# Kernel optimization log

Hardware: AMD Instinct MI355X
Metric: run time of the kernel (lower is better)

Reference implementation:

```python
import jax, jax.numpy as jnp
import numpy as np


def setup_inputs() -> dict:
    key = jax.random.key(0)
    ks = jax.random.split(key, 12)
    B, IN, H = 4096, 512, 1024
    s = lambda k, shape, scale: jax.random.normal(k, shape, dtype=jnp.float32) * scale
    inp = {
        "inputs": s(ks[0], (B, IN), 1.0),
        "h0": s(ks[1], (B, H), 1.0),
        "c0": s(ks[2], (B, H), 1.0),
        "ts": jax.random.uniform(ks[3], (B, 2), dtype=jnp.float32),
        "w_ih": s(ks[4], (4 * H, IN), 1.0 / np.sqrt(IN)),
        "w_hh": s(ks[5], (4 * H, H), 1.0 / np.sqrt(H)),
        "b_ih": s(ks[6], (4 * H,), 1.0 / np.sqrt(H)),
        "b_hh": s(ks[7], (4 * H,), 1.0 / np.sqrt(H)),
        "w1": s(ks[8], (H, H), 1.0 / np.sqrt(H)),
        "b1": s(ks[9], (H,), 1.0 / np.sqrt(H)),
        "w2": s(ks[10], (H, H), 1.0 / np.sqrt(H)),
        "b2": s(ks[11], (H,), 1.0 / np.sqrt(H)),
    }
    return inp


def _lstm_cell(x, h, c, w_ih, w_hh, b_ih, b_hh):
    # gates: [B, 4H] in PyTorch (i, f, g, o) order
    gates = x @ w_ih.T + h @ w_hh.T + b_ih + b_hh
    i, f, g, o = jnp.split(gates, 4, axis=-1)
    i, f, o = jax.nn.sigmoid(i), jax.nn.sigmoid(f), jax.nn.sigmoid(o)
    g = jnp.tanh(g)
    c_new = f * c + i * g
    h_new = o * jnp.tanh(c_new)
    return h_new, c_new


def reference(inputs, h0, c0, ts, w_ih, w_hh, b_ih, b_hh, w1, b1, w2, b2):
    # Two stacked LSTMCell applications sharing the same weights
    h, c = _lstm_cell(inputs, h0, c0, w_ih, w_hh, b_ih, b_hh)
    h, c = _lstm_cell(inputs, h, c, w_ih, w_hh, b_ih, b_hh)

    # Autonomous ODE func: Linear -> Tanh -> Linear
    f = lambda y: jnp.tanh(y @ w1.T + b1) @ w2.T + b2

    # One RK4 step per sample from ts[:,0] to ts[:,1] (batched, no python loop)
    dt = (ts[:, 1] - ts[:, 0])[:, None]  # [B, 1]
    k1 = f(h)
    k2 = f(h + 0.5 * dt * k1)
    k3 = f(h + 0.5 * dt * k2)
    k4 = f(h + dt * k3)
    ht = h + (dt / 6.0) * (k1 + 2.0 * k2 + 2.0 * k3 + k4)
    return (ht, c)
```

## Files before the change

kernel.cpp:

```cpp
#include <hip/hip_runtime.h>

typedef short short8 __attribute__((ext_vector_type(8)));
typedef float f32x4 __attribute__((ext_vector_type(4)));
typedef unsigned short u16x8 __attribute__((ext_vector_type(8)));

#define B_DIM 4096
#define IN_DIM 512
#define H_DIM 1024
#define KCAT 1536

__device__ __forceinline__ float bs2f(unsigned short s) {
    return __uint_as_float(((unsigned int)s) << 16);
}
__device__ __forceinline__ unsigned short f2bs(float f) {
    unsigned int u = __float_as_uint(f);
    u += 0x7fff + ((u >> 16) & 1);
    return (unsigned short)(u >> 16);
}
__device__ __forceinline__ float sigm(float x) { return 1.0f / (1.0f + __expf(-x)); }
__device__ __forceinline__ float ftanh(float x) { return 1.0f - 2.0f / (__expf(2.0f * x) + 1.0f); }

__device__ __forceinline__ int gperm(int r) {
    int g = r >> 10, j = r & 1023;
    return ((j >> 4) << 6) + (g << 4) + (j & 15);
}

#define T0 262144
#define T1 786432
#define T2 1048576
#define T3 1572864
#define T4 1703936
#define T5 1835008
__device__ __forceinline__ u16x8 cvt8(const float* __restrict__ in, long i) {
    float4 a = *(const float4*)(in + i);
    float4 b = *(const float4*)(in + i + 4);
    u16x8 o;
    o[0] = f2bs(a.x); o[1] = f2bs(a.y); o[2] = f2bs(a.z); o[3] = f2bs(a.w);
    o[4] = f2bs(b.x); o[5] = f2bs(b.y); o[6] = f2bs(b.z); o[7] = f2bs(b.w);
    return o;
}
__global__ __launch_bounds__(256) void pack_all(const float* __restrict__ x,
                                                const float* __restrict__ h0,
                                                const float* __restrict__ wih,
                                                const float* __restrict__ whh,
                                                const float* __restrict__ w1,
                                                const float* __restrict__ w2,
                                                unsigned short* __restrict__ xb,
                                                unsigned short* __restrict__ hb0,
                                                unsigned short* __restrict__ wcat,
                                                unsigned short* __restrict__ w116,
                                                unsigned short* __restrict__ w216) {
    long g = (long)blockIdx.x * 256 + threadIdx.x;
    if (g < T0) {
        long i = g * 8;
        *(u16x8*)(xb + i) = cvt8(x, i);
    } else if (g < T1) {
        long i = (g - T0) * 8;
        *(u16x8*)(hb0 + i) = cvt8(h0, i);
    } else if (g < T2) {
        long i = (g - T1) * 8;
        int r = (int)(i / IN_DIM), c = (int)(i % IN_DIM);
        *(u16x8*)(wcat + (size_t)gperm(r) * KCAT + c) = cvt8(wih, i);
    } else if (g < T3) {
        long i = (g - T2) * 8;
        int r = (int)(i / H_DIM), c = (int)(i % H_DIM);
        *(u16x8*)(wcat + (size_t)gperm(r) * KCAT + IN_DIM + c) = cvt8(whh, i);
    } else if (g < T4) {
        long i = (g - T3) * 8;
        *(u16x8*)(w116 + i) = cvt8(w1, i);
    } else if (g < T5) {
        long i = (g - T4) * 8;
        *(u16x8*)(w216 + i) = cvt8(w2, i);
    }
}

__global__ __launch_bounds__(256) void prep_small(const float* __restrict__ bih,
                                                  const float* __restrict__ bhh,
                                                  const float* __restrict__ ts,
                                                  float* __restrict__ bsum,
                                                  float* __restrict__ dtv,
                                                  int n4h, int nb) {
    int i = blockIdx.x * blockDim.x + threadIdx.x;
    if (i < n4h) bsum[gperm(i)] = bih[i] + bhh[i];
    if (i < nb)  dtv[i] = ts[2 * i + 1] - ts[2 * i];
}

#define NT8 (KCAT / 32)

__global__ __launch_bounds__(512) void gemm8(
    const unsigned short* __restrict__ xb,
    const unsigned short* __restrict__ hb,
    const unsigned short* __restrict__ W,
    const float* __restrict__ bias,
    unsigned short* __restrict__ h_out,
    float* __restrict__ c_out,
    const float* __restrict__ c_in) {
    __shared__ unsigned short lA[3][256 * 32];
    __shared__ unsigned short lB[3][256 * 32];
    const int t = threadIdx.x;
    const int lane = t & 63;
    const int wave = t >> 6;
    const int wm = (wave >> 2) * 128;
    const int wn = (wave & 3) * 64;
    const int fr = lane & 15;
    const int kb = lane >> 4;
    const int tile_m = blockIdx.y * 256;
    const int tile_n = blockIdx.x * 256;

    f32x4 acc[8][4];
    #pragma unroll
    for (int i = 0; i < 8; ++i)
        #pragma unroll
        for (int j = 0; j < 4; ++j)
            acc[i][j] = (f32x4){0.f, 0.f, 0.f, 0.f};

    auto stageA = [&](int kt) {
        const int buf = kt % 3;
        #pragma unroll
        for (int j = 0; j < 2; ++j) {
            int idx = j * 512 + t;
            int row = idx >> 2;
            int g = idx & 3;
            int gs = g ^ ((row >> 1) & 3);
            int kk = kt * 32 + gs * 8;
            const unsigned short* src = (kk < IN_DIM)
                ? xb + (size_t)(tile_m + row) * IN_DIM + kk
                : hb + (size_t)(tile_m + row) * H_DIM + (kk - IN_DIM);
            __builtin_amdgcn_global_load_lds(
                (__attribute__((address_space(1))) void*)src,
                (__attribute__((address_space(3))) void*)(&lA[buf][row * 32 + g * 8]), 16, 0, 0);
        }
    };
    auto stageB = [&](int kt) {
        const int buf = kt % 3;
        #pragma unroll
        for (int j = 0; j < 2; ++j) {
            int idx = j * 512 + t;
            int row = idx >> 2;
            int g = idx & 3;
            int gs = g ^ ((row >> 1) & 3);
            int kk = kt * 32 + gs * 8;
            __builtin_amdgcn_global_load_lds(
                (__attribute__((address_space(1))) void*)(W + (size_t)(tile_n + row) * KCAT + kk),
                (__attribute__((address_space(3))) void*)(&lB[buf][row * 32 + g * 8]), 16, 0, 0);
        }
    };

    stageA(0); stageB(0);
    stageA(1); stageB(1);

    for (int kt = 0; kt < NT8; ++kt) {
        const int buf = kt % 3;
        if (kt + 1 < NT8) asm volatile("s_waitcnt vmcnt(4)" ::: "memory");
        else              asm volatile("s_waitcnt vmcnt(0)" ::: "memory");
        __builtin_amdgcn_s_barrier();
        asm volatile("" ::: "memory");
        short8 bfr[4], af[8];
        #pragma unroll
        for (int j = 0; j < 4; ++j) {
            int brow = wn + j * 16 + fr;
            bfr[j] = *(const short8*)&lB[buf][brow * 32 + (kb ^ ((brow >> 1) & 3)) * 8];
        }
        #pragma unroll
        for (int i = 0; i < 8; ++i) {
            int arow = wm + i * 16 + fr;
            af[i] = *(const short8*)&lA[buf][arow * 32 + (kb ^ ((arow >> 1) & 3)) * 8];
        }
        __builtin_amdgcn_s_setprio(1);
        #pragma unroll
        for (int i = 0; i < 8; ++i)
            #pragma unroll
            for (int j = 0; j < 4; ++j)
                acc[i][j] = __builtin_amdgcn_mfma_f32_16x16x32_bf16(af[i], bfr[j], acc[i][j], 0, 0, 0);
        __builtin_amdgcn_s_setprio(0);
        if (kt + 2 < NT8) { stageA(kt + 2); stageB(kt + 2); }
        asm volatile("" ::: "memory");
    }

    const int jbase = ((tile_n + wn) >> 6) << 4;
    float bv[4];
    #pragma unroll
    for (int g = 0; g < 4; ++g) bv[g] = bias[tile_n + wn + g * 16 + fr];
    #pragma unroll
    for (int i = 0; i < 8; ++i) {
        #pragma unroll
        for (int r = 0; r < 4; ++r) {
            const int m = tile_m + wm + i * 16 + kb * 4 + r;
            const int j = jbase + fr;
            float ig = sigm(acc[i][0][r] + bv[0]);
            float fg = sigm(acc[i][1][r] + bv[1]);
            float gg = ftanh(acc[i][2][r] + bv[2]);
            float og = sigm(acc[i][3][r] + bv[3]);
            float cin = c_in[(size_t)m * H_DIM + j];
            float cn = fg * cin + ig * gg;
            float hn = og * ftanh(cn);
            h_out[(size_t)m * H_DIM + j] = f2bs(hn);
            c_out[(size_t)m * H_DIM + j] = cn;
        }
    }
}

#define BKt 32

template <int EPI, int BM, int BN>
__global__ __launch_bounds__(256) void gemm2(
    const unsigned short* __restrict__ A1,
    const unsigned short* __restrict__ W,
    const int M, const int N, const int K,
    const float* __restrict__ bias,
    unsigned short* __restrict__ outb,
    float* __restrict__ outf,
    const unsigned short* __restrict__ hmat,
    const float* __restrict__ dtv,
    float* __restrict__ S,
    unsigned short* __restrict__ ynext,
    const float alpha, const float cw, const int first) {
    constexpr int WM = BM / 2;
    constexpr int WN = BN / 2;
    constexpr int MR = WM / 16;
    constexpr int NR = WN / 16;
    constexpr int ALOADS = BM * BKt / 8 / 256;
    constexpr int BLOADS = BN * BKt / 8 / 256;
    constexpr int LIF = ALOADS + BLOADS;

    __shared__ unsigned short lA[3][BM * BKt];
    __shared__ unsigned short lB[3][BN * BKt];
    const int t = threadIdx.x;
    const int lane = t & 63;
    const int wave = t >> 6;
    const int wm = (wave >> 1) * WM;
    const int wn = (wave & 1) * WN;
    const int fr = lane & 15;
    const int kb = lane >> 4;
    const int tile_m = blockIdx.y * BM;
    const int tile_n = blockIdx.x * BN;

    f32x4 acc[MR][NR];
    #pragma unroll
    for (int i = 0; i < MR; ++i)
        #pragma unroll
        for (int j = 0; j < NR; ++j)
            acc[i][j] = (f32x4){0.f, 0.f, 0.f, 0.f};

    const unsigned short* aptr1 = A1 + (size_t)tile_m * K;
    const unsigned short* wptr  = W + (size_t)tile_n * K;

    auto stage = [&](int kt) {
        const int buf = kt % 3;
        const int k0 = kt * BKt;
        #pragma unroll
        for (int j = 0; j < ALOADS; ++j) {
            int idx = j * 256 + t;
            int row = idx >> 2;
            int col = ((idx & 3) ^ ((row >> 1) & 3)) * 8;
            __builtin_amdgcn_global_load_lds(
                (__attribute__((address_space(1))) void*)(aptr1 + (size_t)row * K + k0 + col),
                (__attribute__((address_space(3))) void*)(&lA[buf][idx * 8]), 16, 0, 0);
        }
        #pragma unroll
        for (int j = 0; j < BLOADS; ++j) {
            int idx = j * 256 + t;
            int row = idx >> 2;
            int col = ((idx & 3) ^ ((row >> 1) & 3)) * 8;
            __builtin_amdgcn_global_load_lds(
                (__attribute__((address_space(1))) void*)(wptr + (size_t)row * K + k0 + col),
                (__attribute__((address_space(3))) void*)(&lB[buf][idx * 8]), 16, 0, 0);
        }
    };

    const int NT = K / BKt;
    stage(0);
    if (NT > 1) stage(1);
    for (int kt = 0; kt < NT; ++kt) {
        const int buf = kt % 3;
        if (kt + 1 < NT) {
            if constexpr (LIF == 2) asm volatile("s_waitcnt vmcnt(2)" ::: "memory");
            else if constexpr (LIF == 3) asm volatile("s_waitcnt vmcnt(3)" ::: "memory");
            else if constexpr (LIF == 4) asm volatile("s_waitcnt vmcnt(4)" ::: "memory");
            else asm volatile("s_waitcnt vmcnt(0)" ::: "memory");
        } else {
            asm volatile("s_waitcnt vmcnt(0)" ::: "memory");
        }
        __builtin_amdgcn_s_barrier();
        asm volatile("" ::: "memory");
        short8 af[MR], bfr[NR];
        #pragma unroll
        for (int i = 0; i < MR; ++i) {
            const int arow = wm + i * 16 + fr;
            af[i] = *(const short8*)&lA[buf][arow * BKt + (kb ^ ((arow >> 1) & 3)) * 8];
        }
        #pragma unroll
        for (int j = 0; j < NR; ++j) {
            const int brow = wn + j * 16 + fr;
            bfr[j] = *(const short8*)&lB[buf][brow * BKt + (kb ^ ((brow >> 1) & 3)) * 8];
        }
        #pragma unroll
        for (int i = 0; i < MR; ++i)
            #pragma unroll
            for (int j = 0; j < NR; ++j)
                acc[i][j] = __builtin_amdgcn_mfma_f32_16x16x32_bf16(af[i], bfr[j], acc[i][j], 0, 0, 0);
        if (kt + 2 < NT) stage(kt + 2);
        asm volatile("" ::: "memory");
    }

    #pragma unroll
    for (int i = 0; i < MR; ++i) {
        #pragma unroll
        for (int r = 0; r < 4; ++r) {
            const int m = tile_m + wm + i * 16 + kb * 4 + r;
            float dt = 0.f;
            if (EPI >= 2) dt = dtv[m];
            #pragma unroll
            for (int j = 0; j < NR; ++j) {
                const int n = tile_n + wn + j * 16 + fr;
                const size_t off = (size_t)m * N + n;
                float v = acc[i][j][r];
                if (bias) v += bias[n];
                if (EPI == 1) {
                    outb[off] = f2bs(ftanh(v));
                } else if (EPI == 2) {
                    float hv = bs2f(hmat[off]);
                    float s = first ? 0.f : S[off];
                    S[off] = s + cw * v;
                    ynext[off] = f2bs(hv + alpha * dt * v);
                } else {
                    float hv = bs2f(hmat[off]);
                    outf[off] = hv + (dt * (1.0f / 6.0f)) * (S[off] + v);
                }
            }
        }
    }
}

extern "C" void kernel_launch(void* const* d_in, const int* in_sizes, int n_in,
                              void* d_out, int out_size, void* d_ws, size_t ws_size,
                              hipStream_t stream) {
    int IX = 0, IH0 = 1, IC0 = 2, ITS = 3, IWIH = 4, IWHH = 5, IBIH = 6, IBHH = 7,
        IW1 = 8, IB1 = 9, IW2 = 10, IB2 = 11;
    const bool sorted_ok = n_in >= 12 &&
        in_sizes[0] == 1024 && in_sizes[1] == 1024 && in_sizes[2] == 4096 &&
        in_sizes[3] == 4096 && in_sizes[4] == 4194304 && in_sizes[5] == 4194304 &&
        in_sizes[6] == 2097152 && in_sizes[7] == 8192 && in_sizes[8] == 1048576 &&
        in_sizes[9] == 1048576 && in_sizes[10] == 4194304 && in_sizes[11] == 2097152;
    if (sorted_ok) {
        IB1 = 0; IB2 = 1; IBHH = 2; IBIH = 3; IC0 = 4; IH0 = 5;
        IX = 6; ITS = 7; IW1 = 8; IW2 = 9; IWHH = 10; IWIH = 11;
    }
    const float* x_f   = (const float*)d_in[IX];
    const float* h0_f  = (const float*)d_in[IH0];
    const float* c0_f  = (const float*)d_in[IC0];
    const float* ts_f  = (const float*)d_in[ITS];
    const float* wih_f = (const float*)d_in[IWIH];
    const float* whh_f = (const float*)d_in[IWHH];
    const float* bih_f = (const float*)d_in[IBIH];
    const float* bhh_f = (const float*)d_in[IBHH];
    const float* w1_f  = (const float*)d_in[IW1];
    const float* b1_f  = (const float*)d_in[IB1];
    const float* w2_f  = (const float*)d_in[IW2];
    const float* b2_f  = (const float*)d_in[IB2];

    constexpr size_t SZ_BIN  = (size_t)B_DIM * IN_DIM;
    constexpr size_t SZ_BH   = (size_t)B_DIM * H_DIM;
    constexpr size_t SZ_HH   = (size_t)H_DIM * H_DIM;
    constexpr size_t SZ_WCAT = (size_t)4 * H_DIM * KCAT;

    float* bsum = (float*)d_ws;
    float* dtv  = bsum + 4 * H_DIM;
    float* S    = dtv + B_DIM;
    float* c1f  = S + SZ_BH;
    unsigned short* wcat = (unsigned short*)(c1f + SZ_BH);
    unsigned short* w116 = wcat + SZ_WCAT;
    unsigned short* w216 = w116 + SZ_HH;
    unsigned short* xb   = w216 + SZ_HH;
    unsigned short* hb0  = xb + SZ_BIN;
    unsigned short* hb1  = hb0 + SZ_BH;
    unsigned short* hb2  = hb1 + SZ_BH;
    unsigned short* ubuf = hb2 + SZ_BH;
    unsigned short* ybuf = ubuf + SZ_BH;

    float* out_ht = (float*)d_out;
    float* out_c  = out_ht + SZ_BH;

    const int TB = 256;
    pack_all<<<T5 / TB, TB, 0, stream>>>(x_f, h0_f, wih_f, whh_f, w1_f, w2_f,
                                         xb, hb0, wcat, w116, w216);
    prep_small<<<(4 * H_DIM) / TB, TB, 0, stream>>>(bih_f, bhh_f, ts_f, bsum, dtv, 4 * H_DIM, B_DIM);

    dim3 g8(4 * H_DIM / 256, B_DIM / 256);
    dim3 gSm(H_DIM / 64, B_DIM / 64);

    gemm8<<<g8, 512, 0, stream>>>(xb, hb0, wcat, bsum, hb1, c1f, c0_f);
    gemm8<<<g8, 512, 0, stream>>>(xb, hb1, wcat, bsum, hb2, out_c, c1f);

    gemm2<1, 64, 64><<<gSm, TB, 0, stream>>>(
        hb2, w116, B_DIM, H_DIM, H_DIM, b1_f,
        ubuf, nullptr, nullptr, nullptr, nullptr, nullptr, 0.f, 0.f, 0);
    gemm2<2, 64, 64><<<gSm, TB, 0, stream>>>(
        ubuf, w216, B_DIM, H_DIM, H_DIM, b2_f,
        nullptr, nullptr, hb2, dtv, S, ybuf, 0.5f, 1.0f, 1);
    gemm2<1, 64, 64><<<gSm, TB, 0, stream>>>(
        ybuf, w116, B_DIM, H_DIM, H_DIM, b1_f,
        ubuf, nullptr, nullptr, nullptr, nullptr, nullptr, 0.f, 0.f, 0);
    gemm2<2, 64, 64><<<gSm, TB, 0, stream>>>(
        ubuf, w216, B_DIM, H_DIM, H_DIM, b2_f,
        nullptr, nullptr, hb2, dtv, S, ybuf, 0.5f, 2.0f, 0);
    gemm2<1, 64, 64><<<gSm, TB, 0, stream>>>(
        ybuf, w116, B_DIM, H_DIM, H_DIM, b1_f,
        ubuf, nullptr, nullptr, nullptr, nullptr, nullptr, 0.f, 0.f, 0);
    gemm2<2, 64, 64><<<gSm, TB, 0, stream>>>(
        ubuf, w216, B_DIM, H_DIM, H_DIM, b2_f,
        nullptr, nullptr, hb2, dtv, S, ybuf, 1.0f, 2.0f, 0);
    gemm2<1, 64, 64><<<gSm, TB, 0, stream>>>(
        ybuf, w116, B_DIM, H_DIM, H_DIM, b1_f,
        ubuf, nullptr, nullptr, nullptr, nullptr, nullptr, 0.f, 0.f, 0);
    gemm2<3, 64, 64><<<gSm, TB, 0, stream>>>(
        ubuf, w216, B_DIM, H_DIM, H_DIM, b2_f,
        nullptr, out_ht, hb2, dtv, S, nullptr, 0.f, 0.f, 0);
}
```

Baseline: 338.8 us.

## Shrink LSTM GEMM M-tile to 128 and rework ODE GEMM to BK=64 double buffering

```diff
diff --git a/kernel.cpp b/kernel.cpp
--- a/kernel.cpp
+++ b/kernel.cpp
@@ -95,41 +95,37 @@
     unsigned short* __restrict__ h_out,
     float* __restrict__ c_out,
     const float* __restrict__ c_in) {
-    __shared__ unsigned short lA[3][256 * 32];
+    __shared__ unsigned short lA[3][128 * 32];
     __shared__ unsigned short lB[3][256 * 32];
     const int t = threadIdx.x;
     const int lane = t & 63;
     const int wave = t >> 6;
-    const int wm = (wave >> 2) * 128;
+    const int wm = (wave >> 2) * 64;
     const int wn = (wave & 3) * 64;
     const int fr = lane & 15;
     const int kb = lane >> 4;
-    const int tile_m = blockIdx.y * 256;
+    const int tile_m = blockIdx.y * 128;
     const int tile_n = blockIdx.x * 256;
 
-    f32x4 acc[8][4];
+    f32x4 acc[4][4];
     #pragma unroll
-    for (int i = 0; i < 8; ++i)
+    for (int i = 0; i < 4; ++i)
         #pragma unroll
         for (int j = 0; j < 4; ++j)
             acc[i][j] = (f32x4){0.f, 0.f, 0.f, 0.f};
 
     auto stageA = [&](int kt) {
         const int buf = kt % 3;
-        #pragma unroll
-        for (int j = 0; j < 2; ++j) {
-            int idx = j * 512 + t;
-            int row = idx >> 2;
-            int g = idx & 3;
-            int gs = g ^ ((row >> 1) & 3);
-            int kk = kt * 32 + gs * 8;
-            const unsigned short* src = (kk < IN_DIM)
-                ? xb + (size_t)(tile_m + row) * IN_DIM + kk
-                : hb + (size_t)(tile_m + row) * H_DIM + (kk - IN_DIM);
-            __builtin_amdgcn_global_load_lds(
-                (__attribute__((address_space(1))) void*)src,
-                (__attribute__((address_space(3))) void*)(&lA[buf][row * 32 + g * 8]), 16, 0, 0);
-        }
+        int row = t >> 2;
+        int g = t & 3;
+        int gs = g ^ ((row >> 1) & 3);
+        int kk = kt * 32 + gs * 8;
+        const unsigned short* src = (kk < IN_DIM)
+            ? xb + (size_t)(tile_m + row) * IN_DIM + kk
+            : hb + (size_t)(tile_m + row) * H_DIM + (kk - IN_DIM);
+        __builtin_amdgcn_global_load_lds(
+            (__attribute__((address_space(1))) void*)src,
+            (__attribute__((address_space(3))) void*)(&lA[buf][row * 32 + g * 8]), 16, 0, 0);
     };
     auto stageB = [&](int kt) {
         const int buf = kt % 3;
@@ -151,24 +147,24 @@
 
     for (int kt = 0; kt < NT8; ++kt) {
         const int buf = kt % 3;
-        if (kt + 1 < NT8) asm volatile("s_waitcnt vmcnt(4)" ::: "memory");
+        if (kt + 1 < NT8) asm volatile("s_waitcnt vmcnt(3)" ::: "memory");
         else              asm volatile("s_waitcnt vmcnt(0)" ::: "memory");
         __builtin_amdgcn_s_barrier();
         asm volatile("" ::: "memory");
-        short8 bfr[4], af[8];
+        short8 bfr[4], af[4];
         #pragma unroll
         for (int j = 0; j < 4; ++j) {
             int brow = wn + j * 16 + fr;
             bfr[j] = *(const short8*)&lB[buf][brow * 32 + (kb ^ ((brow >> 1) & 3)) * 8];
         }
         #pragma unroll
-        for (int i = 0; i < 8; ++i) {
+        for (int i = 0; i < 4; ++i) {
             int arow = wm + i * 16 + fr;
             af[i] = *(const short8*)&lA[buf][arow * 32 + (kb ^ ((arow >> 1) & 3)) * 8];
         }
         __builtin_amdgcn_s_setprio(1);
         #pragma unroll
-        for (int i = 0; i < 8; ++i)
+        for (int i = 0; i < 4; ++i)
             #pragma unroll
             for (int j = 0; j < 4; ++j)
                 acc[i][j] = __builtin_amdgcn_mfma_f32_16x16x32_bf16(af[i], bfr[j], acc[i][j], 0, 0, 0);
@@ -182,7 +178,7 @@
     #pragma unroll
     for (int g = 0; g < 4; ++g) bv[g] = bias[tile_n + wn + g * 16 + fr];
     #pragma unroll
-    for (int i = 0; i < 8; ++i) {
+    for (int i = 0; i < 4; ++i) {
         #pragma unroll
         for (int r = 0; r < 4; ++r) {
             const int m = tile_m + wm + i * 16 + kb * 4 + r;
@@ -200,9 +196,7 @@
     }
 }
 
-#define BKt 32
-
-template <int EPI, int BM, int BN>
+template <int EPI>
 __global__ __launch_bounds__(256) void gemm2(
     const unsigned short* __restrict__ A1,
     const unsigned short* __restrict__ W,
@@ -215,21 +209,15 @@
     float* __restrict__ S,
     unsigned short* __restrict__ ynext,
     const float alpha, const float cw, const int first) {
-    constexpr int WM = BM / 2;
-    constexpr int WN = BN / 2;
-    constexpr int MR = WM / 16;
-    constexpr int NR = WN / 16;
-    constexpr int ALOADS = BM * BKt / 8 / 256;
-    constexpr int BLOADS = BN * BKt / 8 / 256;
-    constexpr int LIF = ALOADS + BLOADS;
-
-    __shared__ unsigned short lA[3][BM * BKt];
-    __shared__ unsigned short lB[3][BN * BKt];
+    constexpr int BM = 64, BN = 64, BK = 64;
+    constexpr int MR = 2, NR = 2;
+    __shared__ unsigned short lA[2][BM * BK];
+    __shared__ unsigned short lB[2][BN * BK];
     const int t = threadIdx.x;
     const int lane = t & 63;
     const int wave = t >> 6;
-    const int wm = (wave >> 1) * WM;
-    const int wn = (wave & 1) * WN;
+    const int wm = (wave >> 1) * 32;
+    const int wn = (wave & 1) * 32;
     const int fr = lane & 15;
     const int kb = lane >> 4;
     const int tile_m = blockIdx.y * BM;
@@ -246,60 +234,61 @@
     const unsigned short* wptr  = W + (size_t)tile_n * K;
 
     auto stage = [&](int kt) {
-        const int buf = kt % 3;
-        const int k0 = kt * BKt;
-        #pragma unroll
-        for (int j = 0; j < ALOADS; ++j) {
+        const int buf = kt & 1;
+        const int k0 = kt * BK;
+        #pragma unroll
+        for (int j = 0; j < 2; ++j) {
             int idx = j * 256 + t;
-            int row = idx >> 2;
-            int col = ((idx & 3) ^ ((row >> 1) & 3)) * 8;
+            int row = idx >> 3;
+            int g = idx & 7;
+            int col = (g ^ (row & 7)) * 8;
             __builtin_amdgcn_global_load_lds(
                 (__attribute__((address_space(1))) void*)(aptr1 + (size_t)row * K + k0 + col),
-                (__attribute__((address_space(3))) void*)(&lA[buf][idx * 8]), 16, 0, 0);
-        }
-        #pragma unroll
-        for (int j = 0; j < BLOADS; ++j) {
+                (__attribute__((address_space(3))) void*)(&lA[buf][row * BK + g * 8]), 16, 0, 0);
+        }
+        #pragma unroll
+        for (int j = 0; j < 2; ++j) {
             int idx = j * 256 + t;
-            int row = idx >> 2;
-            int col = ((idx & 3) ^ ((row >> 1) & 3)) * 8;
+            int row = idx >> 3;
+            int g = idx & 7;
+            int col = (g ^ (row & 7)) * 8;
             __builtin_amdgcn_global_load_lds(
                 (__attribute__((address_space(1))) void*)(wptr + (size_t)row * K + k0 + col),
-                (__attribute__((address_space(3))) void*)(&lB[buf][idx * 8]), 16, 0, 0);
+                (__attribute__((address_space(3))) void*)(&lB[buf][row * BK + g * 8]), 16, 0, 0);
         }
     };
 
-    const int NT = K / BKt;
+    const int NT = K / BK;
     stage(0);
-    if (NT > 1) stage(1);
     for (int kt = 0; kt < NT; ++kt) {
-        const int buf = kt % 3;
-        if (kt + 1 < NT) {
-            if constexpr (LIF == 2) asm volatile("s_waitcnt vmcnt(2)" ::: "memory");
-            else if constexpr (LIF == 3) asm volatile("s_waitcnt vmcnt(3)" ::: "memory");
-            else if constexpr (LIF == 4) asm volatile("s_waitcnt vmcnt(4)" ::: "memory");
-            else asm volatile("s_waitcnt vmcnt(0)" ::: "memory");
-        } else {
-            asm volatile("s_waitcnt vmcnt(0)" ::: "memory");
-        }
+        const int buf = kt & 1;
+        asm volatile("s_waitcnt vmcnt(0)" ::: "memory");
         __builtin_amdgcn_s_barrier();
         asm volatile("" ::: "memory");
-        short8 af[MR], bfr[NR];
-        #pragma unroll
-        for (int i = 0; i < MR; ++i) {
-            const int arow = wm + i * 16 + fr;
-            af[i] = *(const short8*)&lA[buf][arow * BKt + (kb ^ ((arow >> 1) & 3)) * 8];
-        }
-        #pragma unroll
-        for (int j = 0; j < NR; ++j) {
-            const int brow = wn + j * 16 + fr;
-            bfr[j] = *(const short8*)&lB[buf][brow * BKt + (kb ^ ((brow >> 1) & 3)) * 8];
-        }
-        #pragma unroll
-        for (int i = 0; i < MR; ++i)
+        short8 af[2][MR], bfr[2][NR];
+        #pragma unroll
+        for (int h = 0; h < 2; ++h) {
             #pragma unroll
-            for (int j = 0; j < NR; ++j)
-                acc[i][j] = __builtin_amdgcn_mfma_f32_16x16x32_bf16(af[i], bfr[j], acc[i][j], 0, 0, 0);
-        if (kt + 2 < NT) stage(kt + 2);
+            for (int i = 0; i < MR; ++i) {
+                int arow = wm + i * 16 + fr;
+                int gidx = h * 4 + kb;
+                af[h][i] = *(const short8*)&lA[buf][arow * BK + (gidx ^ (arow & 7)) * 8];
+            }
+            #pragma unroll
+            for (int j = 0; j < NR; ++j) {
+                int brow = wn + j * 16 + fr;
+                int gidx = h * 4 + kb;
+                bfr[h][j] = *(const short8*)&lB[buf][brow * BK + (gidx ^ (brow & 7)) * 8];
+            }
+        }
+        if (kt + 1 < NT) stage(kt + 1);
+        #pragma unroll
+        for (int h = 0; h < 2; ++h)
+            #pragma unroll
+            for (int i = 0; i < MR; ++i)
+                #pragma unroll
+                for (int j = 0; j < NR; ++j)
+                    acc[i][j] = __builtin_amdgcn_mfma_f32_16x16x32_bf16(af[h][i], bfr[h][j], acc[i][j], 0, 0, 0);
         asm volatile("" ::: "memory");
     }
 
@@ -386,34 +375,34 @@
                                          xb, hb0, wcat, w116, w216);
     prep_small<<<(4 * H_DIM) / TB, TB, 0, stream>>>(bih_f, bhh_f, ts_f, bsum, dtv, 4 * H_DIM, B_DIM);
 
-    dim3 g8(4 * H_DIM / 256, B_DIM / 256);
+    dim3 g8(4 * H_DIM / 256, B_DIM / 128);
     dim3 gSm(H_DIM / 64, B_DIM / 64);
 
     gemm8<<<g8, 512, 0, stream>>>(xb, hb0, wcat, bsum, hb1, c1f, c0_f);
     gemm8<<<g8, 512, 0, stream>>>(xb, hb1, wcat, bsum, hb2, out_c, c1f);
 
-    gemm2<1, 64, 64><<<gSm, TB, 0, stream>>>(
+    gemm2<1><<<gSm, TB, 0, stream>>>(
         hb2, w116, B_DIM, H_DIM, H_DIM, b1_f,
         ubuf, nullptr, nullptr, nullptr, nullptr, nullptr, 0.f, 0.f, 0);
-    gemm2<2, 64, 64><<<gSm, TB, 0, stream>>>(
+    gemm2<2><<<gSm, TB, 0, stream>>>(
         ubuf, w216, B_DIM, H_DIM, H_DIM, b2_f,
         nullptr, nullptr, hb2, dtv, S, ybuf, 0.5f, 1.0f, 1);
-    gemm2<1, 64, 64><<<gSm, TB, 0, stream>>>(
+    gemm2<1><<<gSm, TB, 0, stream>>>(
         ybuf, w116, B_DIM, H_DIM, H_DIM, b1_f,
         ubuf, nullptr, nullptr, nullptr, nullptr, nullptr, 0.f, 0.f, 0);
-    gemm2<2, 64, 64><<<gSm, TB, 0, stream>>>(
+    gemm2<2><<<gSm, TB, 0, stream>>>(
         ubuf, w216, B_DIM, H_DIM, H_DIM, b2_f,
         nullptr, nullptr, hb2, dtv, S, ybuf, 0.5f, 2.0f, 0);
-    gemm2<1, 64, 64><<<gSm, TB, 0, stream>>>(
+    gemm2<1><<<gSm, TB, 0, stream>>>(
         ybuf, w116, B_DIM, H_DIM, H_DIM, b1_f,
         ubuf, nullptr, nullptr, nullptr, nullptr, nullptr, 0.f, 0.f, 0);
-    gemm2<2, 64, 64><<<gSm, TB, 0, stream>>>(
+    gemm2<2><<<gSm, TB, 0, stream>>>(
         ubuf, w216, B_DIM, H_DIM, H_DIM, b2_f,
         nullptr, nullptr, hb2, dtv, S, ybuf, 1.0f, 2.0f, 0);
-    gemm2<1, 64, 64><<<gSm, TB, 0, stream>>>(
+    gemm2<1><<<gSm, TB, 0, stream>>>(
         ybuf, w116, B_DIM, H_DIM, H_DIM, b1_f,
         ubuf, nullptr, nullptr, nullptr, nullptr, nullptr, 0.f, 0.f, 0);
-    gemm2<3, 64, 64><<<gSm, TB, 0, stream>>>(
+    gemm2<3><<<gSm, TB, 0, stream>>>(
         ubuf, w216, B_DIM, H_DIM, H_DIM, b2_f,
         nullptr, out_ht, hb2, dtv, S, nullptr, 0.f, 0.f, 0);
 }
```

After: 328.9 us. 2.9% less time.
